# Optimization experiments

Hardware: AMD Instinct MI355X
Metric: run time of the kernel (lower is better)

## Reference

```python
import jax, jax.numpy as jnp
import numpy as np

B, T, S, H = 8, 256, 256, 512


def setup_inputs() -> dict:
    key = jax.random.key(0)
    k1, k2, k3, k4, k5, k6, k7 = jax.random.split(key, 7)
    query = jax.random.normal(k1, (B, T, H), dtype=jnp.float32)
    encoder_outputs = jax.random.normal(k2, (B, S, H), dtype=jnp.float32)
    src_lengths = jax.random.randint(k3, (B,), 1, S + 1)
    src_lengths = src_lengths.at[0].set(S)  # ensure max(lengths) == S (torch code masks to lengths.max())
    scale = 1.0 / np.sqrt(H)
    W_s = jax.random.normal(k4, (H, H), dtype=jnp.float32) * scale      # nn.Linear(H,H) weight
    W_h = jax.random.normal(k5, (H, H), dtype=jnp.float32) * scale
    v = jax.random.normal(k6, (H,), dtype=jnp.float32) * scale          # nn.Linear(H,1) weight
    W_out = jax.random.normal(k7, (H, 2 * H), dtype=jnp.float32) * scale  # nn.Linear(2H,H) weight
    return {"query": query, "encoder_outputs": encoder_outputs, "src_lengths": src_lengths,
            "W_s": W_s, "W_h": W_h, "v": v, "W_out": W_out}


def reference(query, encoder_outputs, src_lengths, W_s, W_h, v, W_out):
    # torch Linear: y = x @ W.T
    Ws_q = jnp.einsum('bth,oh->bto', query, W_s)            # (B,T,H)
    Wh_e = jnp.einsum('bsh,oh->bso', encoder_outputs, W_h)  # (B,S,H)
    # score(i,j) = v^T tanh(Ws_q_j + Wh_e_i), broadcast over (B,T,S,H)
    energies = jnp.einsum('btsh,h->bts',
                          jnp.tanh(Ws_q[:, :, None, :] + Wh_e[:, None, :, :]), v)
    mask = jnp.arange(encoder_outputs.shape[1]) < src_lengths[:, None]  # (B,S)
    energies = jnp.where(mask[:, None, :], energies, -jnp.inf)
    attn_weights = jax.nn.softmax(energies, axis=-1)        # (B,T,S)
    context = jnp.einsum('bts,bsh->bth', attn_weights, encoder_outputs)
    combined = jnp.concatenate([context, query], axis=-1)   # (B,T,2H)
    attn_out = jnp.tanh(jnp.einsum('btk,ok->bto', combined, W_out))
    return attn_out
```

## Files before the change

kernel.cpp:

```cpp
#include <hip/hip_runtime.h>
#include <hip/hip_bf16.h>


typedef __attribute__((ext_vector_type(8))) short bf16x8;
typedef __attribute__((ext_vector_type(4))) float floatx4;

#define C2LOG2E 2.8853900817779268f
#define LOG2E   1.4426950408889634f
#define NEGBIG  -1e30f
#define TQ 4

__device__ __forceinline__ float fexp2(float x) { return __builtin_amdgcn_exp2f(x); }
__device__ __forceinline__ float frcp(float x)  { return __builtin_amdgcn_rcpf(x); }
__device__ __forceinline__ float ftanh(float x) {
    return 1.0f - 2.0f * frcp(1.0f + fexp2(C2LOG2E * x));
}
__device__ __forceinline__ float fexp2x(float x) {
    return fexp2(C2LOG2E * x);
}

__device__ __forceinline__ unsigned int f2bf_bits(float f) {
    unsigned int u = __float_as_uint(f);
    return (u + 0x7fffu + ((u >> 16) & 1u)) >> 16;
}

typedef const __attribute__((address_space(1))) unsigned int* gas_u32p;
typedef __attribute__((address_space(3))) unsigned int* las_u32p;
__device__ __forceinline__ void gload16(const void* g, void* l) {
    __builtin_amdgcn_global_load_lds((gas_u32p)g, (las_u32p)l, 16, 0, 0);
}

__global__ __launch_bounds__(256) void cast_all_bf16(
    const float* __restrict__ q,  const float* __restrict__ e,
    const float* __restrict__ Ws, const float* __restrict__ Wh,
    const float* __restrict__ Wo,
    unsigned short* __restrict__ qb,  unsigned short* __restrict__ eb,
    unsigned short* __restrict__ Wsb, unsigned short* __restrict__ Whb,
    unsigned short* __restrict__ Wob)
{
    int blk = blockIdx.x;
    const float* src; unsigned short* dst; int base;
    if      (blk < 1024) { src = q;  dst = qb;  base = blk; }
    else if (blk < 2048) { src = e;  dst = eb;  base = blk - 1024; }
    else if (blk < 2304) { src = Ws; dst = Wsb; base = blk - 2048; }
    else if (blk < 2560) { src = Wh; dst = Whb; base = blk - 2304; }
    else                 { src = Wo; dst = Wob; base = blk - 2560; }
    size_t i = (size_t)base * 1024 + threadIdx.x * 4;
    float4 f = *(const float4*)(src + i);
    ushort4 o;
    o.x = (unsigned short)f2bf_bits(f.x);
    o.y = (unsigned short)f2bf_bits(f.y);
    o.z = (unsigned short)f2bf_bits(f.z);
    o.w = (unsigned short)f2bf_bits(f.w);
    *(ushort4*)(dst + i) = o;
}

__global__ __launch_bounds__(256) void gemm32x64_exp_dual(
    const unsigned short* __restrict__ Xa, const unsigned short* __restrict__ Wa,
    float* __restrict__ Ca,
    const unsigned short* __restrict__ Xb, const unsigned short* __restrict__ Wb_,
    unsigned short* __restrict__ Cbt)
{
    __shared__ unsigned short sA[32 * 64];
    __shared__ unsigned short sB[64 * 64];
    const int K = 512;
    int blk = blockIdx.x;
    bool isA = (blk < 512);
    const unsigned short* X; const unsigned short* W;
    int mt, nt, N;
    if (isA) { X = Xa; W = Wa; N = 512;  mt = blk >> 3; nt = blk & 7; }
    else { blk -= 512; X = Xb; W = Wb_; N = 2048; mt = blk >> 5; nt = blk & 31; }
    int row0 = mt * 32, col0 = nt * 64;
    int tid = threadIdx.x, lane = tid & 63, w = tid >> 6;
    int mw = (w & 1) * 16, nw = (w >> 1) * 32;
    int r = lane & 15;

    int lr  = lane >> 3;
    int csw = ((lane & 7) ^ lr) << 3;
    const unsigned short* gA  = X + (size_t)(row0 + 8 * w + lr) * K + csw;
    const unsigned short* gB0 = W + (size_t)(col0 + 16 * w + lr) * K + csw;
    const unsigned short* gB1 = W + (size_t)(col0 + 16 * w + 8 + lr) * K + csw;
    unsigned short* lA  = &sA[w * 512];
    unsigned short* lB0 = &sB[w * 1024];
    unsigned short* lB1 = &sB[w * 1024 + 512];

    int xr = (r & 7) << 4;
    int cq = (lane >> 4) << 4;
    const char* cA = (const char*)sA;
    const char* cB = (const char*)sB;
    int a0 = (mw + r) * 128 + (cq ^ xr);
    int a1 = (mw + r) * 128 + ((cq + 64) ^ xr);
    int b0 = (nw + r) * 128 + (cq ^ xr);
    int b1 = (nw + r) * 128 + ((cq + 64) ^ xr);

    floatx4 acc0 = {0,0,0,0}, acc1 = {0,0,0,0};
    gload16(gA, lA); gload16(gB0, lB0); gload16(gB1, lB1);

    for (int kb = 0; kb < 8; ++kb) {
        __syncthreads();
        bf16x8 af0 = *(const bf16x8*)(cA + a0);
        bf16x8 af1 = *(const bf16x8*)(cA + a1);
        bf16x8 b00 = *(const bf16x8*)(cB + b0);
        bf16x8 b10 = *(const bf16x8*)(cB + b0 + 2048);
        bf16x8 b01 = *(const bf16x8*)(cB + b1);
        bf16x8 b11 = *(const bf16x8*)(cB + b1 + 2048);
        acc0 = __builtin_amdgcn_mfma_f32_16x16x32_bf16(af0, b00, acc0, 0, 0, 0);
        acc1 = __builtin_amdgcn_mfma_f32_16x16x32_bf16(af0, b10, acc1, 0, 0, 0);
        acc0 = __builtin_amdgcn_mfma_f32_16x16x32_bf16(af1, b01, acc0, 0, 0, 0);
        acc1 = __builtin_amdgcn_mfma_f32_16x16x32_bf16(af1, b11, acc1, 0, 0, 0);
        if (kb < 7) {
            __syncthreads();
            gA += 64; gB0 += 64; gB1 += 64;
            gload16(gA, lA); gload16(gB0, lB0); gload16(gB1, lB1);
        }
    }
    int rq = (lane >> 4) * 4;
    if (isA) {
        float* cp = Ca + (size_t)(row0 + mw + rq) * N + col0 + nw + r;
#pragma unroll
        for (int i = 0; i < 4; ++i) {
            cp[(size_t)i * N]      = fexp2x(acc0[i]);
            cp[(size_t)i * N + 16] = fexp2x(acc1[i]);
        }
    } else {
        unsigned short* cp = Cbt + (size_t)(row0 + mw + rq) * N + col0 + nw + r;
#pragma unroll
        for (int i = 0; i < 4; ++i) {
            cp[(size_t)i * N]      = (unsigned short)f2bf_bits(fexp2x(acc0[i]));
            cp[(size_t)i * N + 16] = (unsigned short)f2bf_bits(fexp2x(acc1[i]));
        }
    }
}

__global__ __launch_bounds__(512) void energies_v11(
    const float* __restrict__ EA,
    const unsigned short* __restrict__ EBT,
    const float* __restrict__ Vv,
    const int* __restrict__ Len,
    float* __restrict__ E)
{
    __shared__ float sA[TQ][516];
    __shared__ float sWn[512];
    __shared__ __align__(16) float sRed[8][TQ][130];

    int tid  = threadIdx.x;
    int lane = tid & 63;
    int w    = tid >> 6;
    int blk  = blockIdx.x;
    int b    = blk >> 7;
    int j    = (blk >> 6) & 1;
    int tq   = blk & 63;
    int len  = Len[b];
    if (j * 128 >= len) return;
    int row0g = b * 256 + tq * TQ;

    {
        int t = tid >> 7, c = (tid & 127) * 4;
        *(float4*)&sA[t][c] = *(const float4*)(EA + (size_t)(row0g + t) * 512 + c);
        sWn[tid] = -2.0f * Vv[tid];
    }
    __syncthreads();

    int h0 = w * 64;
    float acc[TQ][2] = {{0.f}};
    const unsigned short* bt = EBT + (size_t)h0 * 2048 + b * 256 + j * 128 + 2 * lane;

    unsigned int B4[4], P4[4];
#pragma unroll
    for (int i = 0; i < 4; ++i) B4[i] = *(const unsigned int*)(bt + (size_t)i * 2048);
#pragma unroll
    for (int hh = 0; hh < 64; hh += 4) {
        if (hh + 4 < 64) {
            const unsigned short* nb = bt + (size_t)(hh + 4) * 2048;
#pragma unroll
            for (int i = 0; i < 4; ++i) P4[i] = *(const unsigned int*)(nb + (size_t)i * 2048);
        }
        float bl[4], bh[4];
#pragma unroll
        for (int i = 0; i < 4; ++i) {
            bl[i] = __uint_as_float(B4[i] << 16);
            bh[i] = __uint_as_float(B4[i] & 0xffff0000u);
        }
        float4 w4 = *(const float4*)&sWn[h0 + hh];
#pragma unroll
        for (int t = 0; t < TQ; ++t) {
            float4 a4 = *(const float4*)&sA[t][h0 + hh];
            {
                float d0 = fmaf(a4.x, bl[0], 1.0f);
                float d1 = fmaf(a4.y, bl[1], 1.0f);
                float d2 = fmaf(a4.z, bl[2], 1.0f);
                float d3 = fmaf(a4.w, bl[3], 1.0f);
                float num01 = fmaf(w4.x, d1, w4.y * d0);
                float num23 = fmaf(w4.z, d3, w4.w * d2);
                acc[t][0] = fmaf(num01, frcp(d0 * d1), acc[t][0]);
                acc[t][0] = fmaf(num23, frcp(d2 * d3), acc[t][0]);
            }
            {
                float d0 = fmaf(a4.x, bh[0], 1.0f);
                float d1 = fmaf(a4.y, bh[1], 1.0f);
                float d2 = fmaf(a4.z, bh[2], 1.0f);
                float d3 = fmaf(a4.w, bh[3], 1.0f);
                float num01 = fmaf(w4.x, d1, w4.y * d0);
                float num23 = fmaf(w4.z, d3, w4.w * d2);
                acc[t][1] = fmaf(num01, frcp(d0 * d1), acc[t][1]);
                acc[t][1] = fmaf(num23, frcp(d2 * d3), acc[t][1]);
            }
        }
#pragma unroll
        for (int i = 0; i < 4; ++i) B4[i] = P4[i];
    }

#pragma unroll
    for (int t = 0; t < TQ; ++t) {
        float2 av = {acc[t][0], acc[t][1]};
        *(float2*)&sRed[w][t][2 * lane] = av;
    }
    __syncthreads();
    {
        int t = tid >> 7, s = tid & 127;
        float sum = 0.f;
#pragma unroll
        for (int ww = 0; ww < 8; ++ww) sum += sRed[ww][t][s];
        E[(size_t)(row0g + t) * 256 + j * 128 + s] = sum;
    }
}

__global__ __launch_bounds__(512) void softmax_ctx_fused(
    const float* __restrict__ E,
    const unsigned short* __restrict__ Eb,
    const int* __restrict__ Len,
    unsigned short* __restrict__ Ctx)
{
    __shared__ unsigned short EncT[64][264];
    __shared__ unsigned short sWb[64][264];
    int tid = threadIdx.x, lane = tid & 63, w = tid >> 6;
    int blk = blockIdx.x;
    int b = blk & 7, hq = (blk >> 3) & 7, tg = blk >> 6;
    int len = Len[b];

    {
        int s = tid >> 1, hg = (tid & 1) * 32;
        const ushort4* src = (const ushort4*)(Eb + (size_t)(b * 256 + s) * 512 + hq * 64 + hg);
#pragma unroll
        for (int k = 0; k < 8; ++k) {
            ushort4 u = src[k];
            EncT[hg + k * 4 + 0][s] = u.x;
            EncT[hg + k * 4 + 1][s] = u.y;
            EncT[hg + k * 4 + 2][s] = u.z;
            EncT[hg + k * 4 + 3][s] = u.w;
        }
    }
    for (int i = 0; i < 8; ++i) {
        int row = w * 8 + i;
        const float* erow = E + (size_t)(b * 256 + tg * 64 + row) * 256;
        float ev[4];
#pragma unroll
        for (int j = 0; j < 4; ++j) {
            int s = lane + 64 * j;
            ev[j] = (s < len) ? erow[s] : NEGBIG;
        }
        float m = fmaxf(fmaxf(ev[0], ev[1]), fmaxf(ev[2], ev[3]));
#pragma unroll
        for (int o = 1; o < 64; o <<= 1) m = fmaxf(m, __shfl_xor(m, o, 64));
        float wv[4], wsum = 0.f;
#pragma unroll
        for (int j = 0; j < 4; ++j) { wv[j] = fexp2((ev[j] - m) * LOG2E); wsum += wv[j]; }
#pragma unroll
        for (int o = 1; o < 64; o <<= 1) wsum += __shfl_xor(wsum, o, 64);
        float inv = frcp(wsum);
#pragma unroll
        for (int j = 0; j < 4; ++j)
            sWb[row][lane + 64 * j] = (unsigned short)f2bf_bits(wv[j] * inv);
    }
    __syncthreads();

    int mt = w & 3, npair = w >> 2;
    int t0 = mt * 16;
    int r  = lane & 15, kq = (lane >> 4) * 8;
    int n0 = npair * 32 + r;
    floatx4 acc0 = {0.f,0.f,0.f,0.f}, acc1 = {0.f,0.f,0.f,0.f};
#pragma unroll
    for (int k = 0; k < 8; ++k) {
        bf16x8 a  = *(const bf16x8*)(&sWb[t0 + r][kq + 32 * k]);
        bf16x8 b0 = *(const bf16x8*)(&EncT[n0][kq + 32 * k]);
        bf16x8 b1 = *(const bf16x8*)(&EncT[n0 + 16][kq + 32 * k]);
        acc0 = __builtin_amdgcn_mfma_f32_16x16x32_bf16(a, b0, acc0, 0, 0, 0);
        acc1 = __builtin_amdgcn_mfma_f32_16x16x32_bf16(a, b1, acc1, 0, 0, 0);
    }
    int row0 = (lane >> 4) * 4;
    unsigned short* op = Ctx + (size_t)(b * 256 + tg * 64 + t0 + row0) * 512 + hq * 64 + npair * 32 + r;
#pragma unroll
    for (int i = 0; i < 4; ++i) {
        op[i * 512]      = (unsigned short)f2bf_bits(acc0[i]);
        op[i * 512 + 16] = (unsigned short)f2bf_bits(acc1[i]);
    }
}

__global__ __launch_bounds__(256) void out_gemm32x64_tanh(
    const unsigned short* __restrict__ Ctx, const unsigned short* __restrict__ Q,
    const unsigned short* __restrict__ Wout, float* __restrict__ Out)
{
    __shared__ unsigned short sA[32 * 64];
    __shared__ unsigned short sB[64 * 64];
    const int N = 512, KW = 1024;
    int blk = blockIdx.x;
    int mt = blk >> 3, nt = blk & 7;
    int row0 = mt * 32, col0 = nt * 64;
    int tid = threadIdx.x, lane = tid & 63, w = tid >> 6;
    int mw = (w & 1) * 16, nw = (w >> 1) * 32;
    int r = lane & 15;

    int lr  = lane >> 3;
    int csw = ((lane & 7) ^ lr) << 3;
    const unsigned short* gactx = Ctx  + (size_t)(row0 + 8 * w + lr) * 512 + csw;
    const unsigned short* gaq   = Q    + (size_t)(row0 + 8 * w + lr) * 512 + csw;
    const unsigned short* gB0   = Wout + (size_t)(col0 + 16 * w + lr) * KW + csw;
    const unsigned short* gB1   = Wout + (size_t)(col0 + 16 * w + 8 + lr) * KW + csw;
    unsigned short* lA  = &sA[w * 512];
    unsigned short* lB0 = &sB[w * 1024];
    unsigned short* lB1 = &sB[w * 1024 + 512];

    int xr = (r & 7) << 4;
    int cq = (lane >> 4) << 4;
    const char* cA = (const char*)sA;
    const char* cB = (const char*)sB;
    int a0 = (mw + r) * 128 + (cq ^ xr);
    int a1 = (mw + r) * 128 + ((cq + 64) ^ xr);
    int b0 = (nw + r) * 128 + (cq ^ xr);
    int b1 = (nw + r) * 128 + ((cq + 64) ^ xr);

    floatx4 acc0 = {0,0,0,0}, acc1 = {0,0,0,0};
    gload16(gactx, lA); gload16(gB0, lB0); gload16(gB1, lB1);

    for (int kb = 0; kb < 16; ++kb) {
        __syncthreads();
        bf16x8 af0 = *(const bf16x8*)(cA + a0);
        bf16x8 af1 = *(const bf16x8*)(cA + a1);
        bf16x8 b00 = *(const bf16x8*)(cB + b0);
        bf16x8 b10 = *(const bf16x8*)(cB + b0 + 2048);
        bf16x8 b01 = *(const bf16x8*)(cB + b1);
        bf16x8 b11 = *(const bf16x8*)(cB + b1 + 2048);
        acc0 = __builtin_amdgcn_mfma_f32_16x16x32_bf16(af0, b00, acc0, 0, 0, 0);
        acc1 = __builtin_amdgcn_mfma_f32_16x16x32_bf16(af0, b10, acc1, 0, 0, 0);
        acc0 = __builtin_amdgcn_mfma_f32_16x16x32_bf16(af1, b01, acc0, 0, 0, 0);
        acc1 = __builtin_amdgcn_mfma_f32_16x16x32_bf16(af1, b11, acc1, 0, 0, 0);
        if (kb < 15) {
            __syncthreads();
            int kn = kb + 1;
            const unsigned short* ga = (kn < 8 ? gactx : gaq) + (kn & 7) * 64;
            gB0 += 64; gB1 += 64;
            gload16(ga, lA); gload16(gB0, lB0); gload16(gB1, lB1);
        }
    }
    int rq = (lane >> 4) * 4;
    float* op = Out + (size_t)(row0 + mw + rq) * N + col0 + nw + r;
#pragma unroll
    for (int i = 0; i < 4; ++i) {
        op[(size_t)i * N]      = ftanh(acc0[i]);
        op[(size_t)i * N + 16] = ftanh(acc1[i]);
    }
}

extern "C" void kernel_launch(void* const* d_in, const int* in_sizes, int n_in,
                              void* d_out, int out_size, void* d_ws, size_t ws_size,
                              hipStream_t stream)
{
    const float* query = (const float*)d_in[0];
    const float* enc   = (const float*)d_in[1];
    const int*   len   = (const int*)d_in[2];
    const float* Ws    = (const float*)d_in[3];
    const float* Wh    = (const float*)d_in[4];
    const float* v     = (const float*)d_in[5];
    const float* Wout  = (const float*)d_in[6];
    float* out = (float*)d_out;

    float* EA   = (float*)d_ws;
    float* E    = EA + 2048 * 512;
    unsigned short* EBTb = (unsigned short*)(E + 2048 * 256);
    unsigned short* qb  = EBTb + 512 * 2048;
    unsigned short* eb  = qb + 2048 * 512;
    unsigned short* Wsb = eb + 2048 * 512;
    unsigned short* Whb = Wsb + 512 * 512;
    unsigned short* Wob = Whb + 512 * 512;
    unsigned short* ctx = Wob + 512 * 1024;

    cast_all_bf16<<<3072, 256, 0, stream>>>(query, enc, Ws, Wh, Wout,
                                            qb, eb, Wsb, Whb, Wob);
    gemm32x64_exp_dual<<<1024, 256, 0, stream>>>(qb, Wsb, EA, Whb, eb, EBTb);
    energies_v11<<<1024, 512, 0, stream>>>(EA, EBTb, v, len, E);
    softmax_ctx_fused<<<256, 512, 0, stream>>>(E, eb, len, ctx);
    out_gemm32x64_tanh<<<512, 256, 0, stream>>>(ctx, qb, Wob, out);
}
```

Before: 120.4 us.

## Split energies kernel over hidden halves with 8 query rows per block

The energies kernel now gives each block 8 query rows instead of 4 and only half of the hidden dimension (32 h per warp instead of 64), so each bf16 encoder-term load is reused across twice as many query rows. The two hidden-half partial sums go to separate buffers E0 and E1, and the softmax kernel adds them when it reads. This cuts global traffic for the encoder-term matrix per unit of work, at the cost of one extra energy buffer to write and read and more accumulator registers.

```diff
diff --git a/kernel.cpp b/kernel.cpp
--- a/kernel.cpp
+++ b/kernel.cpp
@@ -8,7 +8,6 @@
 #define C2LOG2E 2.8853900817779268f
 #define LOG2E   1.4426950408889634f
 #define NEGBIG  -1e30f
-#define TQ 4
 
 __device__ __forceinline__ float fexp2(float x) { return __builtin_amdgcn_exp2f(x); }
 __device__ __forceinline__ float frcp(float x)  { return __builtin_amdgcn_rcpf(x); }
@@ -132,16 +131,18 @@
     }
 }
 
-__global__ __launch_bounds__(512) void energies_v11(
+#define TQ8 8
+__global__ __launch_bounds__(512) void energies_v13(
     const float* __restrict__ EA,
     const unsigned short* __restrict__ EBT,
     const float* __restrict__ Vv,
     const int* __restrict__ Len,
-    float* __restrict__ E)
-{
-    __shared__ float sA[TQ][516];
-    __shared__ float sWn[512];
-    __shared__ __align__(16) float sRed[8][TQ][130];
+    float* __restrict__ E0,
+    float* __restrict__ E1)
+{
+    __shared__ float sA[TQ8][260];
+    __shared__ float sWn[256];
+    __shared__ __align__(16) float sRed[8][TQ8][130];
 
     int tid  = threadIdx.x;
     int lane = tid & 63;
@@ -149,28 +150,32 @@
     int blk  = blockIdx.x;
     int b    = blk >> 7;
     int j    = (blk >> 6) & 1;
-    int tq   = blk & 63;
+    int hf   = (blk >> 5) & 1;
+    int tq   = blk & 31;
     int len  = Len[b];
     if (j * 128 >= len) return;
-    int row0g = b * 256 + tq * TQ;
+    int row0g = b * 256 + tq * TQ8;
 
     {
-        int t = tid >> 7, c = (tid & 127) * 4;
-        *(float4*)&sA[t][c] = *(const float4*)(EA + (size_t)(row0g + t) * 512 + c);
-        sWn[tid] = -2.0f * Vv[tid];
+        int t = tid >> 6, c = (tid & 63) * 4;
+        *(float4*)&sA[t][c] = *(const float4*)(EA + (size_t)(row0g + t) * 512 + hf * 256 + c);
+        if (tid < 256) sWn[tid] = -2.0f * Vv[hf * 256 + tid];
     }
     __syncthreads();
 
-    int h0 = w * 64;
-    float acc[TQ][2] = {{0.f}};
-    const unsigned short* bt = EBT + (size_t)h0 * 2048 + b * 256 + j * 128 + 2 * lane;
+    int h0 = w * 32;
+    float acc[TQ8][2];
+#pragma unroll
+    for (int t = 0; t < TQ8; ++t) { acc[t][0] = 0.f; acc[t][1] = 0.f; }
+    const unsigned short* bt = EBT + (size_t)(hf * 256 + h0) * 2048
+                                   + b * 256 + j * 128 + 2 * lane;
 
     unsigned int B4[4], P4[4];
 #pragma unroll
     for (int i = 0; i < 4; ++i) B4[i] = *(const unsigned int*)(bt + (size_t)i * 2048);
 #pragma unroll
-    for (int hh = 0; hh < 64; hh += 4) {
-        if (hh + 4 < 64) {
+    for (int hh = 0; hh < 32; hh += 4) {
+        if (hh + 4 < 32) {
             const unsigned short* nb = bt + (size_t)(hh + 4) * 2048;
 #pragma unroll
             for (int i = 0; i < 4; ++i) P4[i] = *(const unsigned int*)(nb + (size_t)i * 2048);
@@ -183,7 +188,7 @@
         }
         float4 w4 = *(const float4*)&sWn[h0 + hh];
 #pragma unroll
-        for (int t = 0; t < TQ; ++t) {
+        for (int t = 0; t < TQ8; ++t) {
             float4 a4 = *(const float4*)&sA[t][h0 + hh];
             {
                 float d0 = fmaf(a4.x, bl[0], 1.0f);
@@ -211,22 +216,28 @@
     }
 
 #pragma unroll
-    for (int t = 0; t < TQ; ++t) {
+    for (int t = 0; t < TQ8; ++t) {
         float2 av = {acc[t][0], acc[t][1]};
         *(float2*)&sRed[w][t][2 * lane] = av;
     }
     __syncthreads();
     {
-        int t = tid >> 7, s = tid & 127;
-        float sum = 0.f;
-#pragma unroll
-        for (int ww = 0; ww < 8; ++ww) sum += sRed[ww][t][s];
-        E[(size_t)(row0g + t) * 256 + j * 128 + s] = sum;
+        int s = tid & 127;
+        float* Ep = hf ? E1 : E0;
+#pragma unroll
+        for (int half = 0; half < 2; ++half) {
+            int t = (tid >> 7) + 4 * half;
+            float sum = 0.f;
+#pragma unroll
+            for (int ww = 0; ww < 8; ++ww) sum += sRed[ww][t][s];
+            Ep[(size_t)(row0g + t) * 256 + j * 128 + s] = sum;
+        }
     }
 }
 
 __global__ __launch_bounds__(512) void softmax_ctx_fused(
-    const float* __restrict__ E,
+    const float* __restrict__ E0,
+    const float* __restrict__ E1,
     const unsigned short* __restrict__ Eb,
     const int* __restrict__ Len,
     unsigned short* __restrict__ Ctx)
@@ -252,12 +263,14 @@
     }
     for (int i = 0; i < 8; ++i) {
         int row = w * 8 + i;
-        const float* erow = E + (size_t)(b * 256 + tg * 64 + row) * 256;
+        size_t ro = (size_t)(b * 256 + tg * 64 + row) * 256;
+        const float* er0 = E0 + ro;
+        const float* er1 = E1 + ro;
         float ev[4];
 #pragma unroll
         for (int j = 0; j < 4; ++j) {
             int s = lane + 64 * j;
-            ev[j] = (s < len) ? erow[s] : NEGBIG;
+            ev[j] = (s < len) ? (er0[s] + er1[s]) : NEGBIG;
         }
         float m = fmaxf(fmaxf(ev[0], ev[1]), fmaxf(ev[2], ev[3]));
 #pragma unroll
@@ -375,8 +388,9 @@
     float* out = (float*)d_out;
 
     float* EA   = (float*)d_ws;
-    float* E    = EA + 2048 * 512;
-    unsigned short* EBTb = (unsigned short*)(E + 2048 * 256);
+    float* E0   = EA + 2048 * 512;
+    float* E1   = E0 + 2048 * 256;
+    unsigned short* EBTb = (unsigned short*)(E1 + 2048 * 256);
     unsigned short* qb  = EBTb + 512 * 2048;
     unsigned short* eb  = qb + 2048 * 512;
     unsigned short* Wsb = eb + 2048 * 512;
@@ -387,7 +401,7 @@
     cast_all_bf16<<<3072, 256, 0, stream>>>(query, enc, Ws, Wh, Wout,
                                             qb, eb, Wsb, Whb, Wob);
     gemm32x64_exp_dual<<<1024, 256, 0, stream>>>(qb, Wsb, EA, Whb, eb, EBTb);
-    energies_v11<<<1024, 512, 0, stream>>>(EA, EBTb, v, len, E);
-    softmax_ctx_fused<<<256, 512, 0, stream>>>(E, eb, len, ctx);
+    energies_v13<<<1024, 512, 0, stream>>>(EA, EBTb, v, len, E0, E1);
+    softmax_ctx_fused<<<256, 512, 0, stream>>>(E0, E1, eb, len, ctx);
     out_gemm32x64_tanh<<<512, 256, 0, stream>>>(ctx, qb, Wob, out);
 }
```

Result: slower. 130.3 us (+8.2%).
